# Performance work log

Hardware: AMD Instinct MI355X
Metric: run time of the kernel (lower is better)

## Reference

```python
import jax, jax.numpy as jnp
import numpy as np
from jax import lax

N_BITS = 4
SIGNED = True
P0 = 1e-3
QN = -2 ** (N_BITS - 1)          # -8
QP = 2 ** (N_BITS - 1) - 1       # 7
SHAPE = (8192, 8192)


def setup_inputs() -> dict:
    key = jax.random.key(0)
    kx, ke = jax.random.split(key)
    x = jax.random.normal(kx, SHAPE, dtype=jnp.float32)
    # epsilon: per-element, per-bit Bernoulli(p0) flips packed into an integer
    # (bits @ 2**arange(N_bits)), exactly as sample_noise() does.
    n = int(np.prod(SHAPE))
    bits = jax.random.bernoulli(ke, P0, (n, N_BITS)).astype(jnp.int32)
    bw = (2 ** jnp.arange(N_BITS)).astype(jnp.int32)
    epsilon = bits @ bw                      # [n] in [0, 2**N_bits)
    q_range = jnp.float32(1.0)               # nn.Parameter init value
    return {"x": x, "q_range": q_range, "epsilon": epsilon}


def _int2bin(v):
    # signed int -> unsigned two's complement in N_BITS bits
    return jnp.where(v < 0, v + 2 ** N_BITS, v)


def _bin2int(u):
    # unsigned two's complement -> signed int
    mask = 2 ** (N_BITS - 1) - 1             # 0b0111
    return -(u & ~mask) + (u & mask)


def reference(x, q_range, epsilon):
    sg = lax.stop_gradient
    # grad_scale STE on q_range (use_grad_scaled=True)
    gs = 1.0 / jnp.sqrt(jnp.float32(x.size))
    qr = sg(q_range - q_range * gs) + q_range * gs
    # _Clamp: symmetric clip (signed=True)
    xc = jnp.clip(x, -qr, qr)
    step = sg(qr) / 2 ** (N_BITS - 1)        # step_size, detached
    xi = xc / step                           # zero_point = 0
    # round_pass STE
    xr = sg(jnp.round(xi) - xi) + xi
    # clamp-to-range STE
    xcl = jnp.clip(xr, QN, QP)
    x_int = sg(xcl - xr) + xr                # float, integer-valued
    # inject_noise: XOR bit flips on the two's-complement representation
    u = _int2bin(sg(x_int).astype(jnp.int32)).reshape(-1)
    up = u ^ epsilon
    pert = _bin2int(up).astype(jnp.float32).reshape(x.shape)
    x_noisy = pert + x_int - sg(x_int)       # STE: noise is a constant offset
    # linear_dequantize
    return x_noisy * step
```

## Files before the change

kernel.cpp:

```cpp
#include <hip/hip_runtime.h>


typedef float f32x4 __attribute__((ext_vector_type(4)));
typedef int   i32x4 __attribute__((ext_vector_type(4)));

#define UNROLL 4
#define BLOCK  256
#define TILE   (BLOCK * UNROLL)

__device__ __forceinline__ float qn_elem(float x, int e, float qr,
                                         float step, float inv_step) {
    float xc = fminf(fmaxf(x, -qr), qr);
    float xr = rintf(xc * inv_step);
    xr = fminf(fmaxf(xr, -8.0f), 7.0f);
    int u    = ((int)xr) & 15;
    int up   = u ^ e;
    int pert = (up << 28) >> 28;
    return (float)pert * step;
}

__global__ __launch_bounds__(BLOCK) void WCAT_quantnoise_kernel(
    const f32x4* __restrict__ x4,
    const i32x4* __restrict__ e4,
    const float* __restrict__ q_range_p,
    f32x4* __restrict__ out4,
    int n4)
{
    const float qr       = q_range_p[0];
    const float step     = qr * 0.125f;
    const float inv_step = 8.0f / qr;

    const int tid    = threadIdx.x;
    const int ntiles = n4 / TILE;

    for (int t = blockIdx.x; t < ntiles; t += gridDim.x) {
        const int base = t * TILE + tid;

        f32x4 xv[UNROLL];
        i32x4 ev[UNROLL];
#pragma unroll
        for (int k = 0; k < UNROLL; ++k) {
            xv[k] = x4[base + k * BLOCK];
            ev[k] = e4[base + k * BLOCK];
        }
        __builtin_amdgcn_sched_barrier(0);

#pragma unroll
        for (int k = 0; k < UNROLL; ++k) {
            f32x4 ov;
#pragma unroll
            for (int c = 0; c < 4; ++c)
                ov[c] = qn_elem(xv[k][c], ev[k][c], qr, step, inv_step);
            out4[base + k * BLOCK] = ov;
        }
    }

    for (int i = ntiles * TILE + blockIdx.x * BLOCK + tid; i < n4;
         i += gridDim.x * BLOCK) {
        f32x4 xv = x4[i];
        i32x4 ev = e4[i];
        f32x4 ov;
#pragma unroll
        for (int c = 0; c < 4; ++c)
            ov[c] = qn_elem(xv[c], ev[c], qr, step, inv_step);
        out4[i] = ov;
    }
}

extern "C" void kernel_launch(void* const* d_in, const int* in_sizes, int n_in,
                              void* d_out, int out_size, void* d_ws, size_t ws_size,
                              hipStream_t stream) {
    const float* x       = (const float*)d_in[0];
    const float* q_range = (const float*)d_in[1];
    const int*   epsilon = (const int*)d_in[2];
    float*       out     = (float*)d_out;

    const int n  = in_sizes[0];
    const int n4 = n / 4;

    int grid = 2048;
    int ntiles = n4 / TILE;
    if (grid > ntiles && ntiles > 0) grid = ntiles;

    WCAT_quantnoise_kernel<<<grid, BLOCK, 0, stream>>>(
        (const f32x4*)x, (const i32x4*)epsilon, q_range, (f32x4*)out, n4);
}
```

Measured before the change: 580.6 us.

## Double-buffer input loads through LDS with direct global-to-LDS copies

Replaces register-staged unrolled loads with per-wave double-buffered global_load_lds copies into shared memory, prefetching the next tile while the current one is computed and stored. The aim is to keep memory requests in flight continuously for this bandwidth-bound elementwise kernel. It adds LDS traffic, manual vmcnt waits and a smaller per-iteration tile, and it relies on the 16-byte global_load_lds path being supported and correctly ordered without explicit barriers.

```diff
diff --git a/kernel.cpp b/kernel.cpp
--- a/kernel.cpp
+++ b/kernel.cpp
@@ -4,9 +4,10 @@
 typedef float f32x4 __attribute__((ext_vector_type(4)));
 typedef int   i32x4 __attribute__((ext_vector_type(4)));
 
-#define UNROLL 4
-#define BLOCK  256
-#define TILE   (BLOCK * UNROLL)
+#define BLOCK   256
+#define WAVES   4
+#define PW      2
+#define TILE_F4 (BLOCK * PW)
 
 __device__ __forceinline__ float qn_elem(float x, int e, float qr,
                                          float step, float inv_step) {
@@ -19,6 +20,15 @@
     return (float)pert * step;
 }
 
+__device__ __forceinline__ f32x4 qn_vec4(f32x4 xv, i32x4 ev, float qr,
+                                         float step, float inv_step) {
+    f32x4 ov;
+#pragma unroll
+    for (int c = 0; c < 4; ++c)
+        ov[c] = qn_elem(xv[c], ev[c], qr, step, inv_step);
+    return ov;
+}
+
 __global__ __launch_bounds__(BLOCK) void WCAT_quantnoise_kernel(
     const f32x4* __restrict__ x4,
     const i32x4* __restrict__ e4,
@@ -26,44 +36,71 @@
     f32x4* __restrict__ out4,
     int n4)
 {
+    __shared__ f32x4 lx[2][WAVES][PW * 64];
+    __shared__ i32x4 le[2][WAVES][PW * 64];
+
     const float qr       = q_range_p[0];
     const float step     = qr * 0.125f;
     const float inv_step = 8.0f / qr;
 
-    const int tid    = threadIdx.x;
-    const int ntiles = n4 / TILE;
+    const int tid  = threadIdx.x;
+    const int wid  = tid >> 6;
+    const int lane = tid & 63;
 
-    for (int t = blockIdx.x; t < ntiles; t += gridDim.x) {
-        const int base = t * TILE + tid;
+    const int NT     = n4 / TILE_F4;
+    const int stride = gridDim.x;
 
-        f32x4 xv[UNROLL];
-        i32x4 ev[UNROLL];
+    int t   = blockIdx.x;
+    int buf = 0;
+
+    if (t < NT) {
 #pragma unroll
-        for (int k = 0; k < UNROLL; ++k) {
-            xv[k] = x4[base + k * BLOCK];
-            ev[k] = e4[base + k * BLOCK];
+        for (int j = 0; j < PW; ++j) {
+            const f32x4* gx = x4 + (size_t)t * TILE_F4 + wid * (PW * 64) + j * 64 + lane;
+            const i32x4* ge = e4 + (size_t)t * TILE_F4 + wid * (PW * 64) + j * 64 + lane;
+            __builtin_amdgcn_global_load_lds(
+                (const __attribute__((address_space(1))) void*)gx,
+                (__attribute__((address_space(3))) void*)&lx[0][wid][j * 64], 16, 0, 0);
+            __builtin_amdgcn_global_load_lds(
+                (const __attribute__((address_space(1))) void*)ge,
+                (__attribute__((address_space(3))) void*)&le[0][wid][j * 64], 16, 0, 0);
+        }
+    }
+
+    for (; t < NT; t += stride) {
+        const int tn = t + stride;
+        if (tn < NT) {
+            const int nb = buf ^ 1;
+#pragma unroll
+            for (int j = 0; j < PW; ++j) {
+                const f32x4* gx = x4 + (size_t)tn * TILE_F4 + wid * (PW * 64) + j * 64 + lane;
+                const i32x4* ge = e4 + (size_t)tn * TILE_F4 + wid * (PW * 64) + j * 64 + lane;
+                __builtin_amdgcn_global_load_lds(
+                    (const __attribute__((address_space(1))) void*)gx,
+                    (__attribute__((address_space(3))) void*)&lx[nb][wid][j * 64], 16, 0, 0);
+                __builtin_amdgcn_global_load_lds(
+                    (const __attribute__((address_space(1))) void*)ge,
+                    (__attribute__((address_space(3))) void*)&le[nb][wid][j * 64], 16, 0, 0);
+            }
+            asm volatile("s_waitcnt vmcnt(4)" ::: "memory");
+        } else {
+            asm volatile("s_waitcnt vmcnt(0)" ::: "memory");
         }
         __builtin_amdgcn_sched_barrier(0);
 
 #pragma unroll
-        for (int k = 0; k < UNROLL; ++k) {
-            f32x4 ov;
-#pragma unroll
-            for (int c = 0; c < 4; ++c)
-                ov[c] = qn_elem(xv[k][c], ev[k][c], qr, step, inv_step);
-            out4[base + k * BLOCK] = ov;
+        for (int j = 0; j < PW; ++j) {
+            f32x4 xv = lx[buf][wid][j * 64 + lane];
+            i32x4 ev = le[buf][wid][j * 64 + lane];
+            out4[(size_t)t * TILE_F4 + wid * (PW * 64) + j * 64 + lane] =
+                qn_vec4(xv, ev, qr, step, inv_step);
         }
+        buf ^= 1;
     }
 
-    for (int i = ntiles * TILE + blockIdx.x * BLOCK + tid; i < n4;
+    for (int i = NT * TILE_F4 + blockIdx.x * BLOCK + tid; i < n4;
          i += gridDim.x * BLOCK) {
-        f32x4 xv = x4[i];
-        i32x4 ev = e4[i];
-        f32x4 ov;
-#pragma unroll
-        for (int c = 0; c < 4; ++c)
-            ov[c] = qn_elem(xv[c], ev[c], qr, step, inv_step);
-        out4[i] = ov;
+        out4[i] = qn_vec4(x4[i], e4[i], qr, step, inv_step);
     }
 }
 
@@ -78,9 +115,10 @@
     const int n  = in_sizes[0];
     const int n4 = n / 4;
 
+    const int NT = n4 / TILE_F4;
     int grid = 2048;
-    int ntiles = n4 / TILE;
-    if (grid > ntiles && ntiles > 0) grid = ntiles;
+    if (grid > NT && NT > 0) grid = NT;
+    if (NT == 0) grid = 1;
 
     WCAT_quantnoise_kernel<<<grid, BLOCK, 0, stream>>>(
         (const f32x4*)x, (const i32x4*)epsilon, q_range, (f32x4*)out, n4);
```

After: 586.0 us. No clear change (+0.9%).
